# Optimization experiments

Measured on AMD Instinct MI355X. Metric: run time of the kernel, lower is better.

The kernel has to match this reference:

```python
import jax, jax.numpy as jnp
import numpy as np

EPS = float(np.finfo(np.float32).eps)  # torch.finfo(float32).eps


def _inv2x2(M):
    """Elementwise inverse of 2x2 complex matrices. M: (..., 2, 2) complex."""
    det = M[..., 0, 0] * M[..., 1, 1] - M[..., 0, 1] * M[..., 1, 0]
    # matches torch _inv: conj(z) / |z|^2
    inv_det = jnp.conj(det) / (jnp.abs(det) ** 2)
    row0 = jnp.stack([inv_det * M[..., 1, 1], -inv_det * M[..., 0, 1]], axis=-1)
    row1 = jnp.stack([-inv_det * M[..., 1, 0], inv_det * M[..., 0, 0]], axis=-1)
    return jnp.stack([row0, row1], axis=-2)


def _em(y, x, iterations):
    # y: (F, B, C, 2, S) real/imag; x: (F, B, C, 2)
    yc = y[..., 0, :] + 1j * y[..., 1, :]          # (F, B, C, S) complex
    xc = x[..., 0] + 1j * x[..., 1]                # (F, B, C)   complex
    nb_channels = yc.shape[2]
    reg = jnp.sqrt(jnp.asarray(EPS, jnp.float32)) * jnp.eye(
        nb_channels, dtype=yc.dtype)               # sqrt(eps)*I regularizer
    v = jnp.mean(jnp.abs(yc) ** 2, axis=2)         # (F, B, S)
    R = jnp.einsum('fbcs,fbds->bcds', yc, jnp.conj(yc))
    for _ in range(iterations):
        # E-step: PSD = channel-average power spectrogram
        v = jnp.mean(jnp.abs(yc) ** 2, axis=2)     # (F, B, S)
        # spatial covariance: sum_f y y^H / (eps + sum_f v)  -> (B, C, C, S)
        R = jnp.einsum('fbcs,fbds->bcds', yc, jnp.conj(yc))
        R = R / (EPS + jnp.sum(v, axis=0))[:, None, None, :]
        # mixture covariance Cxx = sqrt(eps)*I + sum_j v_j R_j  -> (F, B, C, C)
        Cxx = reg[None, None] + jnp.einsum('fbs,bcds->fbcd', v, R)
        inv_Cxx = _inv2x2(Cxx)
        # Wiener gain G_j = v_j * R_j @ inv_Cxx  -> (F, B, C, C, S)
        gain = jnp.einsum('fbs,bcks,fbkd->fbcds', v, R, inv_Cxx)
        # apply filter: y_j = G_j @ x
        yc = jnp.einsum('fbcds,fbd->fbcs', gain, xc)
    y_out = jnp.stack([jnp.real(yc), jnp.imag(yc)], axis=-2)   # (F, B, C, 2, S)
    R_out = jnp.stack([jnp.real(R), jnp.imag(R)], axis=-2)     # (B, C, C, 2, S)
    return y_out, v, R_out


def setup_inputs() -> dict:
    key = jax.random.key(0)
    k1, k2 = jax.random.split(key)
    F, B, C, S = 1000, 2049, 2, 4
    y = jax.random.normal(k1, (F, B, C, 2, S), dtype=jnp.float32)
    x = jax.random.normal(k2, (F, B, C, 2), dtype=jnp.float32)
    return {"y": y, "x": x, "iterations": 2}


def reference(y, x, iterations):
    return _em(y, x, iterations)
```

## Files before the change

### kernel.cpp

```cpp
#include <hip/hip_runtime.h>

#define FDIM 1000
#define BDIM 2049
#define NTH  256
#define NF   4

#define V_OFF 32784000ull
#define R_OFF 40980000ull

__global__ __launch_bounds__(NTH, 2) void Separator_55791625175550_kernel(
    const float* __restrict__ y,
    const float* __restrict__ x,
    const int*   __restrict__ itp,
    float*       __restrict__ out)
{
    const float EPSF = 1.1920928955078125e-07f;
    const float REGC = 3.4526698300124393e-04f;

    const int b    = blockIdx.x;
    const int tid  = threadIdx.x;
    const int lane = tid & 63;
    const int wid  = tid >> 6;

    const int  iters   = itp[0];
    const int  nloops  = (iters > 0) ? iters : 1;
    const bool zero_it = (iters == 0);

    __shared__ float red[4][20];
    __shared__ float rsum[20];
    __shared__ float rnorm[16];

    float y0r[NF][4], y0i[NF][4], y1r[NF][4], y1i[NF][4];
    float xr0[NF], xi0[NF], xr1[NF], xi1[NF];
    float v[NF][4];

    #pragma unroll
    for (int k = 0; k < NF; ++k) {
        const int f = tid + k * NTH;
        if (f < FDIM) {
            const float4* yp = reinterpret_cast<const float4*>(y) + (size_t)(f * BDIM + b) * 4;
            float4 a0 = yp[0];
            float4 a1 = yp[1];
            float4 a2 = yp[2];
            float4 a3 = yp[3];
            y0r[k][0]=a0.x; y0r[k][1]=a0.y; y0r[k][2]=a0.z; y0r[k][3]=a0.w;
            y0i[k][0]=a1.x; y0i[k][1]=a1.y; y0i[k][2]=a1.z; y0i[k][3]=a1.w;
            y1r[k][0]=a2.x; y1r[k][1]=a2.y; y1r[k][2]=a2.z; y1r[k][3]=a2.w;
            y1i[k][0]=a3.x; y1i[k][1]=a3.y; y1i[k][2]=a3.z; y1i[k][3]=a3.w;
            float4 xv = reinterpret_cast<const float4*>(x)[(size_t)(f * BDIM + b)];
            xr0[k]=xv.x; xi0[k]=xv.y; xr1[k]=xv.z; xi1[k]=xv.w;
        } else {
            #pragma unroll
            for (int s = 0; s < 4; ++s) { y0r[k][s]=0.f; y0i[k][s]=0.f; y1r[k][s]=0.f; y1i[k][s]=0.f; }
            xr0[k]=0.f; xi0[k]=0.f; xr1[k]=0.f; xi1[k]=0.f;
        }
    }

    for (int it = 0; it < nloops; ++it) {
        const bool last = (it == nloops - 1);

        float a00[4], a11[4], a01r[4], a01i[4], sv[4];
        #pragma unroll
        for (int s = 0; s < 4; ++s) { a00[s]=0.f; a11[s]=0.f; a01r[s]=0.f; a01i[s]=0.f; sv[s]=0.f; }
        #pragma unroll
        for (int k = 0; k < NF; ++k) {
            #pragma unroll
            for (int s = 0; s < 4; ++s) {
                const float p0 = y0r[k][s]*y0r[k][s] + y0i[k][s]*y0i[k][s];
                const float p1 = y1r[k][s]*y1r[k][s] + y1i[k][s]*y1i[k][s];
                v[k][s] = 0.5f * (p0 + p1);
                a00[s] += p0;
                a11[s] += p1;
                a01r[s] += y0r[k][s]*y1r[k][s] + y0i[k][s]*y1i[k][s];
                a01i[s] += y0i[k][s]*y1r[k][s] - y0r[k][s]*y1i[k][s];
                sv[s]   += v[k][s];
            }
        }

        float vals[20];
        #pragma unroll
        for (int s = 0; s < 4; ++s) {
            vals[s]=a00[s]; vals[4+s]=a11[s]; vals[8+s]=a01r[s]; vals[12+s]=a01i[s]; vals[16+s]=sv[s];
        }
        #pragma unroll
        for (int j = 0; j < 20; ++j) {
            float t = vals[j];
            t += __shfl_xor(t, 1);  t += __shfl_xor(t, 2);  t += __shfl_xor(t, 4);
            t += __shfl_xor(t, 8);  t += __shfl_xor(t, 16); t += __shfl_xor(t, 32);
            vals[j] = t;
        }
        if (lane == 0) {
            #pragma unroll
            for (int j = 0; j < 20; ++j) red[wid][j] = vals[j];
        }
        __syncthreads();
        if (tid < 20) rsum[tid] = red[0][tid] + red[1][tid] + red[2][tid] + red[3][tid];
        __syncthreads();
        if (tid < 16) rnorm[tid] = rsum[tid] / (EPSF + rsum[16 + (tid & 3)]);
        __syncthreads();

        float rn00[4], rn11[4], rn01r[4], rn01i[4];
        #pragma unroll
        for (int s = 0; s < 4; ++s) {
            rn00[s]=rnorm[s]; rn11[s]=rnorm[4+s]; rn01r[s]=rnorm[8+s]; rn01i[s]=rnorm[12+s];
        }

        if (last) {
            #pragma unroll
            for (int k = 0; k < NF; ++k) {
                const int f = tid + k * NTH;
                if (f < FDIM) {
                    float4 vv = make_float4(v[k][0], v[k][1], v[k][2], v[k][3]);
                    *reinterpret_cast<float4*>(out + V_OFF + (size_t)(f * BDIM + b) * 4) = vv;
                }
            }
            if (tid < 32) {
                const int c  = (tid >> 4) & 1;
                const int d  = (tid >> 3) & 1;
                const int ri = (tid >> 2) & 1;
                const int s  = tid & 3;
                const float* src = zero_it ? rsum : rnorm;
                float val;
                if (c == d) val = ri ? 0.0f : src[(c ? 4 : 0) + s];
                else if (c == 0) val = ri ?  src[12 + s] : src[8 + s];
                else             val = ri ? -src[12 + s] : src[8 + s];
                out[R_OFF + (size_t)b * 32 + tid] = val;
            }
        }

        if (!zero_it) {
            #pragma unroll
            for (int k = 0; k < NF; ++k) {
                const int f = tid + k * NTH;
                if (f < FDIM) {
                    float c00 = REGC, c11 = REGC, c01r = 0.f, c01i = 0.f;
                    #pragma unroll
                    for (int s = 0; s < 4; ++s) {
                        c00  += v[k][s] * rn00[s];
                        c11  += v[k][s] * rn11[s];
                        c01r += v[k][s] * rn01r[s];
                        c01i += v[k][s] * rn01i[s];
                    }
                    const float det  = c00 * c11 - (c01r * c01r + c01i * c01i);
                    const float invd = det / (det * det);
                    const float i00 = invd * c11, i11 = invd * c00;
                    const float i01r = -invd * c01r, i01i = -invd * c01i;
                    const float w0r = i00 * xr0[k] + (i01r * xr1[k] - i01i * xi1[k]);
                    const float w0i = i00 * xi0[k] + (i01r * xi1[k] + i01i * xr1[k]);
                    const float w1r = (i01r * xr0[k] + i01i * xi0[k]) + i11 * xr1[k];
                    const float w1i = (i01r * xi0[k] - i01i * xr0[k]) + i11 * xi1[k];
                    #pragma unroll
                    for (int s = 0; s < 4; ++s) {
                        const float vs = v[k][s];
                        y0r[k][s] = vs * (rn00[s] * w0r + (rn01r[s] * w1r - rn01i[s] * w1i));
                        y0i[k][s] = vs * (rn00[s] * w0i + (rn01r[s] * w1i + rn01i[s] * w1r));
                        y1r[k][s] = vs * ((rn01r[s] * w0r + rn01i[s] * w0i) + rn11[s] * w1r);
                        y1i[k][s] = vs * ((rn01r[s] * w0i - rn01i[s] * w0r) + rn11[s] * w1i);
                    }
                }
            }
        }
    }

    #pragma unroll
    for (int k = 0; k < NF; ++k) {
        const int f = tid + k * NTH;
        if (f < FDIM) {
            float4* op = reinterpret_cast<float4*>(out) + (size_t)(f * BDIM + b) * 4;
            op[0] = make_float4(y0r[k][0], y0r[k][1], y0r[k][2], y0r[k][3]);
            op[1] = make_float4(y0i[k][0], y0i[k][1], y0i[k][2], y0i[k][3]);
            op[2] = make_float4(y1r[k][0], y1r[k][1], y1r[k][2], y1r[k][3]);
            op[3] = make_float4(y1i[k][0], y1i[k][1], y1i[k][2], y1i[k][3]);
        }
    }
}

extern "C" void kernel_launch(void* const* d_in, const int* in_sizes, int n_in,
                              void* d_out, int out_size, void* d_ws, size_t ws_size,
                              hipStream_t stream) {
    const float* y   = (const float*)d_in[0];
    const float* x   = (const float*)d_in[1];
    const int*   itp = (const int*)d_in[2];
    float* out = (float*)d_out;
    Separator_55791625175550_kernel<<<BDIM, NTH, 0, stream>>>(y, x, itp, out);
}
```

Measured before the change: 355.7 us.

## Split EM into three tiled kernels with coalesced b-tiles and partial reductions

Replaces the one-block-per-b kernel, whose threads stride across f with large gaps, with three kernels over 16-wide b tiles and 8 f-slices. Neighbouring threads now read contiguous memory. The per-b covariance sums are reduced through workspace partials, and the intermediate estimate is carried as the power v instead of the full y, since each updated y can be rebuilt from v, x and R. This adds two extra launches and extra global round trips for v. The code only handles up to two iterations, so larger iteration counts would be computed incorrectly.

```diff
diff --git a/kernel.cpp b/kernel.cpp
--- a/kernel.cpp
+++ b/kernel.cpp
@@ -3,174 +3,325 @@
 #define FDIM 1000
 #define BDIM 2049
 #define NTH  256
-#define NF   4
+#define FS   8
+#define FT   125
+#define BT   16
+#define NBT  129
+#define GRID (NBT * FS)
 
 #define V_OFF 32784000ull
 #define R_OFF 40980000ull
 
-__global__ __launch_bounds__(NTH, 2) void Separator_55791625175550_kernel(
-    const float* __restrict__ y,
-    const float* __restrict__ x,
-    const int*   __restrict__ itp,
-    float*       __restrict__ out)
+#define P2_OFF ((size_t)BDIM * FS * 20)
+
+#define EPSF 1.1920928955078125e-07f
+#define REGC 3.4526698300124393e-04f
+
+__global__ __launch_bounds__(NTH) void k1_power(
+    const float* __restrict__ y, float* __restrict__ v, float* __restrict__ part1)
 {
-    const float EPSF = 1.1920928955078125e-07f;
-    const float REGC = 3.4526698300124393e-04f;
-
-    const int b    = blockIdx.x;
-    const int tid  = threadIdx.x;
-    const int lane = tid & 63;
-    const int wid  = tid >> 6;
-
-    const int  iters   = itp[0];
-    const int  nloops  = (iters > 0) ? iters : 1;
-    const bool zero_it = (iters == 0);
-
-    __shared__ float red[4][20];
-    __shared__ float rsum[20];
-    __shared__ float rnorm[16];
-
-    float y0r[NF][4], y0i[NF][4], y1r[NF][4], y1i[NF][4];
-    float xr0[NF], xi0[NF], xr1[NF], xi1[NF];
-    float v[NF][4];
-
-    #pragma unroll
-    for (int k = 0; k < NF; ++k) {
-        const int f = tid + k * NTH;
-        if (f < FDIM) {
-            const float4* yp = reinterpret_cast<const float4*>(y) + (size_t)(f * BDIM + b) * 4;
-            float4 a0 = yp[0];
-            float4 a1 = yp[1];
-            float4 a2 = yp[2];
-            float4 a3 = yp[3];
-            y0r[k][0]=a0.x; y0r[k][1]=a0.y; y0r[k][2]=a0.z; y0r[k][3]=a0.w;
-            y0i[k][0]=a1.x; y0i[k][1]=a1.y; y0i[k][2]=a1.z; y0i[k][3]=a1.w;
-            y1r[k][0]=a2.x; y1r[k][1]=a2.y; y1r[k][2]=a2.z; y1r[k][3]=a2.w;
-            y1i[k][0]=a3.x; y1i[k][1]=a3.y; y1i[k][2]=a3.z; y1i[k][3]=a3.w;
-            float4 xv = reinterpret_cast<const float4*>(x)[(size_t)(f * BDIM + b)];
-            xr0[k]=xv.x; xi0[k]=xv.y; xr1[k]=xv.z; xi1[k]=xv.w;
-        } else {
-            #pragma unroll
-            for (int s = 0; s < 4; ++s) { y0r[k][s]=0.f; y0i[k][s]=0.f; y1r[k][s]=0.f; y1i[k][s]=0.f; }
-            xr0[k]=0.f; xi0[k]=0.f; xr1[k]=0.f; xi1[k]=0.f;
-        }
-    }
-
-    for (int it = 0; it < nloops; ++it) {
-        const bool last = (it == nloops - 1);
-
-        float a00[4], a11[4], a01r[4], a01i[4], sv[4];
+    const int btile = blockIdx.x / FS;
+    const int fs    = blockIdx.x % FS;
+    const int tid   = threadIdx.x;
+    const int bs    = tid & 15;
+    const int fi    = tid >> 4;
+    const int wid   = tid >> 6;
+    const int b     = btile * BT + bs;
+    const bool vb   = (b < BDIM);
+
+    float acc[20];
+    #pragma unroll
+    for (int j = 0; j < 20; ++j) acc[j] = 0.f;
+
+    const int f0 = fs * FT;
+    #pragma unroll
+    for (int ii = 0; ii < 8; ++ii) {
+        const int fo = ii * 16 + fi;
+        if (fo < FT && vb) {
+            const int f = f0 + fo;
+            const size_t e = (size_t)f * BDIM + b;
+            const float4* yp = reinterpret_cast<const float4*>(y) + e * 4;
+            float4 a0 = yp[0], a1 = yp[1], a2 = yp[2], a3 = yp[3];
+            float y0r[4] = {a0.x,a0.y,a0.z,a0.w};
+            float y0i[4] = {a1.x,a1.y,a1.z,a1.w};
+            float y1r[4] = {a2.x,a2.y,a2.z,a2.w};
+            float y1i[4] = {a3.x,a3.y,a3.z,a3.w};
+            float vv[4];
+            #pragma unroll
+            for (int s = 0; s < 4; ++s) {
+                const float p0 = y0r[s]*y0r[s] + y0i[s]*y0i[s];
+                const float p1 = y1r[s]*y1r[s] + y1i[s]*y1i[s];
+                vv[s] = 0.5f * (p0 + p1);
+                acc[s]    += p0;
+                acc[4+s]  += p1;
+                acc[8+s]  += y0r[s]*y1r[s] + y0i[s]*y1i[s];
+                acc[12+s] += y0i[s]*y1r[s] - y0r[s]*y1i[s];
+                acc[16+s] += vv[s];
+            }
+            reinterpret_cast<float4*>(v)[e] = make_float4(vv[0], vv[1], vv[2], vv[3]);
+        }
+    }
+    #pragma unroll
+    for (int j = 0; j < 20; ++j) {
+        float t = acc[j];
+        t += __shfl_xor(t, 16);
+        t += __shfl_xor(t, 32);
+        acc[j] = t;
+    }
+    __shared__ float red[4][16][20];
+    if ((tid & 63) < 16) {
         #pragma unroll
-        for (int s = 0; s < 4; ++s) { a00[s]=0.f; a11[s]=0.f; a01r[s]=0.f; a01i[s]=0.f; sv[s]=0.f; }
+        for (int j = 0; j < 20; ++j) red[wid][bs][j] = acc[j];
+    }
+    __syncthreads();
+    for (int idx = tid; idx < 320; idx += NTH) {
+        const int bss = idx & 15, j = idx >> 4;
+        const int bb = btile * BT + bss;
+        if (bb < BDIM)
+            part1[((size_t)bb * FS + fs) * 20 + j] =
+                red[0][bss][j] + red[1][bss][j] + red[2][bss][j] + red[3][bss][j];
+    }
+}
+
+__global__ __launch_bounds__(NTH) void k3_em(
+    const float* __restrict__ x, float* __restrict__ v,
+    const float* __restrict__ part1, float* __restrict__ part2,
+    const int* __restrict__ itp)
+{
+    const int btile = blockIdx.x / FS;
+    const int fs    = blockIdx.x % FS;
+    const int tid   = threadIdx.x;
+    const int bs    = tid & 15;
+    const int fi    = tid >> 4;
+    const int wid   = tid >> 6;
+    const int b     = btile * BT + bs;
+    const bool vb   = (b < BDIM);
+    const int iters = itp[0];
+
+    __shared__ float rsumS[16][20];
+    __shared__ float rnormS[16][16];
+    for (int idx = tid; idx < 320; idx += NTH) {
+        const int bss = idx & 15, j = idx >> 4;
+        const int bb = btile * BT + bss;
+        float s = 0.f;
+        if (bb < BDIM) {
+            #pragma unroll
+            for (int q = 0; q < FS; ++q) s += part1[((size_t)bb * FS + q) * 20 + j];
+        }
+        rsumS[bss][j] = s;
+    }
+    __syncthreads();
+    {
+        const int bss = tid & 15, j = tid >> 4;
+        rnormS[bss][j] = rsumS[bss][j] / (EPSF + rsumS[bss][16 + (j & 3)]);
+    }
+    __syncthreads();
+
+    if (iters <= 1) {
+        for (int idx = tid; idx < 320; idx += NTH) {
+            const int bss = idx & 15, j = idx >> 4;
+            const int bb = btile * BT + bss;
+            if (bb < BDIM)
+                part2[((size_t)bb * FS + fs) * 20 + j] = (fs == 0) ? rsumS[bss][j] : 0.f;
+        }
+        return;
+    }
+
+    float rn00[4], rn11[4], rn01r[4], rn01i[4];
+    #pragma unroll
+    for (int s = 0; s < 4; ++s) {
+        rn00[s]=rnormS[bs][s]; rn11[s]=rnormS[bs][4+s];
+        rn01r[s]=rnormS[bs][8+s]; rn01i[s]=rnormS[bs][12+s];
+    }
+
+    float acc[20];
+    #pragma unroll
+    for (int j = 0; j < 20; ++j) acc[j] = 0.f;
+
+    const int f0 = fs * FT;
+    #pragma unroll
+    for (int ii = 0; ii < 8; ++ii) {
+        const int fo = ii * 16 + fi;
+        if (fo < FT && vb) {
+            const int f = f0 + fo;
+            const size_t e = (size_t)f * BDIM + b;
+            float4 vv4 = reinterpret_cast<const float4*>(v)[e];
+            float4 xv  = reinterpret_cast<const float4*>(x)[e];
+            float v1[4] = {vv4.x, vv4.y, vv4.z, vv4.w};
+            float c00 = REGC, c11 = REGC, c01r = 0.f, c01i = 0.f;
+            #pragma unroll
+            for (int s = 0; s < 4; ++s) {
+                c00  += v1[s]*rn00[s];
+                c11  += v1[s]*rn11[s];
+                c01r += v1[s]*rn01r[s];
+                c01i += v1[s]*rn01i[s];
+            }
+            const float det  = c00*c11 - (c01r*c01r + c01i*c01i);
+            const float invd = det / (det*det);
+            const float i00 = invd*c11, i11 = invd*c00;
+            const float i01r = -invd*c01r, i01i = -invd*c01i;
+            const float xr0 = xv.x, xi0 = xv.y, xr1 = xv.z, xi1 = xv.w;
+            const float w0r = i00*xr0 + (i01r*xr1 - i01i*xi1);
+            const float w0i = i00*xi0 + (i01r*xi1 + i01i*xr1);
+            const float w1r = (i01r*xr0 + i01i*xi0) + i11*xr1;
+            const float w1i = (i01r*xi0 - i01i*xr0) + i11*xi1;
+            float v2[4];
+            #pragma unroll
+            for (int s = 0; s < 4; ++s) {
+                const float vs = v1[s];
+                const float y0r = vs*(rn00[s]*w0r + (rn01r[s]*w1r - rn01i[s]*w1i));
+                const float y0i = vs*(rn00[s]*w0i + (rn01r[s]*w1i + rn01i[s]*w1r));
+                const float y1r = vs*((rn01r[s]*w0r + rn01i[s]*w0i) + rn11[s]*w1r);
+                const float y1i = vs*((rn01r[s]*w0i - rn01i[s]*w0r) + rn11[s]*w1i);
+                const float p0 = y0r*y0r + y0i*y0i;
+                const float p1 = y1r*y1r + y1i*y1i;
+                v2[s] = 0.5f*(p0 + p1);
+                acc[s]    += p0;
+                acc[4+s]  += p1;
+                acc[8+s]  += y0r*y1r + y0i*y1i;
+                acc[12+s] += y0i*y1r - y0r*y1i;
+                acc[16+s] += v2[s];
+            }
+            reinterpret_cast<float4*>(v)[e] = make_float4(v2[0], v2[1], v2[2], v2[3]);
+        }
+    }
+    #pragma unroll
+    for (int j = 0; j < 20; ++j) {
+        float t = acc[j];
+        t += __shfl_xor(t, 16);
+        t += __shfl_xor(t, 32);
+        acc[j] = t;
+    }
+    __shared__ float red[4][16][20];
+    if ((tid & 63) < 16) {
         #pragma unroll
-        for (int k = 0; k < NF; ++k) {
-            #pragma unroll
-            for (int s = 0; s < 4; ++s) {
-                const float p0 = y0r[k][s]*y0r[k][s] + y0i[k][s]*y0i[k][s];
-                const float p1 = y1r[k][s]*y1r[k][s] + y1i[k][s]*y1i[k][s];
-                v[k][s] = 0.5f * (p0 + p1);
-                a00[s] += p0;
-                a11[s] += p1;
-                a01r[s] += y0r[k][s]*y1r[k][s] + y0i[k][s]*y1i[k][s];
-                a01i[s] += y0i[k][s]*y1r[k][s] - y0r[k][s]*y1i[k][s];
-                sv[s]   += v[k][s];
-            }
-        }
-
-        float vals[20];
+        for (int j = 0; j < 20; ++j) red[wid][bs][j] = acc[j];
+    }
+    __syncthreads();
+    for (int idx = tid; idx < 320; idx += NTH) {
+        const int bss = idx & 15, j = idx >> 4;
+        const int bb = btile * BT + bss;
+        if (bb < BDIM)
+            part2[((size_t)bb * FS + fs) * 20 + j] =
+                red[0][bss][j] + red[1][bss][j] + red[2][bss][j] + red[3][bss][j];
+    }
+}
+
+__global__ __launch_bounds__(NTH) void k5_final(
+    const float* __restrict__ y, const float* __restrict__ x, const float* __restrict__ v,
+    const float* __restrict__ part2, float* __restrict__ yout, float* __restrict__ Rout,
+    const int* __restrict__ itp)
+{
+    const int btile = blockIdx.x / FS;
+    const int fs    = blockIdx.x % FS;
+    const int tid   = threadIdx.x;
+    const int bs    = tid & 15;
+    const int fi    = tid >> 4;
+    const int b     = btile * BT + bs;
+    const bool vb   = (b < BDIM);
+    const int iters = itp[0];
+
+    __shared__ float rsumS[16][20];
+    __shared__ float rnormS[16][16];
+    for (int idx = tid; idx < 320; idx += NTH) {
+        const int bss = idx & 15, j = idx >> 4;
+        const int bb = btile * BT + bss;
+        float s = 0.f;
+        if (bb < BDIM) {
+            #pragma unroll
+            for (int q = 0; q < FS; ++q) s += part2[((size_t)bb * FS + q) * 20 + j];
+        }
+        rsumS[bss][j] = s;
+    }
+    __syncthreads();
+    {
+        const int bss = tid & 15, j = tid >> 4;
+        rnormS[bss][j] = rsumS[bss][j] / (EPSF + rsumS[bss][16 + (j & 3)]);
+    }
+    __syncthreads();
+
+    if (fs == 0) {
+        for (int idx = tid; idx < 512; idx += NTH) {
+            const int bss = idx >> 5, r = idx & 31;
+            const int bb = btile * BT + bss;
+            if (bb < BDIM) {
+                const int c = (r>>4)&1, d = (r>>3)&1, ri = (r>>2)&1, s = r&3;
+                const bool raw = (iters == 0);
+                float val;
+                if (c == d) {
+                    val = ri ? 0.f : (raw ? rsumS[bss][(c?4:0)+s] : rnormS[bss][(c?4:0)+s]);
+                } else {
+                    const float re = raw ? rsumS[bss][8+s]  : rnormS[bss][8+s];
+                    const float im = raw ? rsumS[bss][12+s] : rnormS[bss][12+s];
+                    val = ri ? (c == 0 ? im : -im) : re;
+                }
+                Rout[(size_t)bb * 32 + r] = val;
+            }
+        }
+    }
+
+    const int f0 = fs * FT;
+    if (iters == 0) {
         #pragma unroll
-        for (int s = 0; s < 4; ++s) {
-            vals[s]=a00[s]; vals[4+s]=a11[s]; vals[8+s]=a01r[s]; vals[12+s]=a01i[s]; vals[16+s]=sv[s];
-        }
-        #pragma unroll
-        for (int j = 0; j < 20; ++j) {
-            float t = vals[j];
-            t += __shfl_xor(t, 1);  t += __shfl_xor(t, 2);  t += __shfl_xor(t, 4);
-            t += __shfl_xor(t, 8);  t += __shfl_xor(t, 16); t += __shfl_xor(t, 32);
-            vals[j] = t;
-        }
-        if (lane == 0) {
-            #pragma unroll
-            for (int j = 0; j < 20; ++j) red[wid][j] = vals[j];
-        }
-        __syncthreads();
-        if (tid < 20) rsum[tid] = red[0][tid] + red[1][tid] + red[2][tid] + red[3][tid];
-        __syncthreads();
-        if (tid < 16) rnorm[tid] = rsum[tid] / (EPSF + rsum[16 + (tid & 3)]);
-        __syncthreads();
-
-        float rn00[4], rn11[4], rn01r[4], rn01i[4];
-        #pragma unroll
-        for (int s = 0; s < 4; ++s) {
-            rn00[s]=rnorm[s]; rn11[s]=rnorm[4+s]; rn01r[s]=rnorm[8+s]; rn01i[s]=rnorm[12+s];
-        }
-
-        if (last) {
-            #pragma unroll
-            for (int k = 0; k < NF; ++k) {
-                const int f = tid + k * NTH;
-                if (f < FDIM) {
-                    float4 vv = make_float4(v[k][0], v[k][1], v[k][2], v[k][3]);
-                    *reinterpret_cast<float4*>(out + V_OFF + (size_t)(f * BDIM + b) * 4) = vv;
-                }
-            }
-            if (tid < 32) {
-                const int c  = (tid >> 4) & 1;
-                const int d  = (tid >> 3) & 1;
-                const int ri = (tid >> 2) & 1;
-                const int s  = tid & 3;
-                const float* src = zero_it ? rsum : rnorm;
-                float val;
-                if (c == d) val = ri ? 0.0f : src[(c ? 4 : 0) + s];
-                else if (c == 0) val = ri ?  src[12 + s] : src[8 + s];
-                else             val = ri ? -src[12 + s] : src[8 + s];
-                out[R_OFF + (size_t)b * 32 + tid] = val;
-            }
-        }
-
-        if (!zero_it) {
-            #pragma unroll
-            for (int k = 0; k < NF; ++k) {
-                const int f = tid + k * NTH;
-                if (f < FDIM) {
-                    float c00 = REGC, c11 = REGC, c01r = 0.f, c01i = 0.f;
-                    #pragma unroll
-                    for (int s = 0; s < 4; ++s) {
-                        c00  += v[k][s] * rn00[s];
-                        c11  += v[k][s] * rn11[s];
-                        c01r += v[k][s] * rn01r[s];
-                        c01i += v[k][s] * rn01i[s];
-                    }
-                    const float det  = c00 * c11 - (c01r * c01r + c01i * c01i);
-                    const float invd = det / (det * det);
-                    const float i00 = invd * c11, i11 = invd * c00;
-                    const float i01r = -invd * c01r, i01i = -invd * c01i;
-                    const float w0r = i00 * xr0[k] + (i01r * xr1[k] - i01i * xi1[k]);
-                    const float w0i = i00 * xi0[k] + (i01r * xi1[k] + i01i * xr1[k]);
-                    const float w1r = (i01r * xr0[k] + i01i * xi0[k]) + i11 * xr1[k];
-                    const float w1i = (i01r * xi0[k] - i01i * xr0[k]) + i11 * xi1[k];
-                    #pragma unroll
-                    for (int s = 0; s < 4; ++s) {
-                        const float vs = v[k][s];
-                        y0r[k][s] = vs * (rn00[s] * w0r + (rn01r[s] * w1r - rn01i[s] * w1i));
-                        y0i[k][s] = vs * (rn00[s] * w0i + (rn01r[s] * w1i + rn01i[s] * w1r));
-                        y1r[k][s] = vs * ((rn01r[s] * w0r + rn01i[s] * w0i) + rn11[s] * w1r);
-                        y1i[k][s] = vs * ((rn01r[s] * w0i - rn01i[s] * w0r) + rn11[s] * w1i);
-                    }
-                }
-            }
-        }
-    }
-
-    #pragma unroll
-    for (int k = 0; k < NF; ++k) {
-        const int f = tid + k * NTH;
-        if (f < FDIM) {
-            float4* op = reinterpret_cast<float4*>(out) + (size_t)(f * BDIM + b) * 4;
-            op[0] = make_float4(y0r[k][0], y0r[k][1], y0r[k][2], y0r[k][3]);
-            op[1] = make_float4(y0i[k][0], y0i[k][1], y0i[k][2], y0i[k][3]);
-            op[2] = make_float4(y1r[k][0], y1r[k][1], y1r[k][2], y1r[k][3]);
-            op[3] = make_float4(y1i[k][0], y1i[k][1], y1i[k][2], y1i[k][3]);
+        for (int ii = 0; ii < 8; ++ii) {
+            const int fo = ii * 16 + fi;
+            if (fo < FT && vb) {
+                const size_t e = (size_t)(f0 + fo) * BDIM + b;
+                const float4* yp = reinterpret_cast<const float4*>(y) + e * 4;
+                float4* op = reinterpret_cast<float4*>(yout) + e * 4;
+                op[0] = yp[0]; op[1] = yp[1]; op[2] = yp[2]; op[3] = yp[3];
+            }
+        }
+        return;
+    }
+
+    float rn00[4], rn11[4], rn01r[4], rn01i[4];
+    #pragma unroll
+    for (int s = 0; s < 4; ++s) {
+        rn00[s]=rnormS[bs][s]; rn11[s]=rnormS[bs][4+s];
+        rn01r[s]=rnormS[bs][8+s]; rn01i[s]=rnormS[bs][12+s];
+    }
+
+    #pragma unroll
+    for (int ii = 0; ii < 8; ++ii) {
+        const int fo = ii * 16 + fi;
+        if (fo < FT && vb) {
+            const int f = f0 + fo;
+            const size_t e = (size_t)f * BDIM + b;
+            float4 vv4 = reinterpret_cast<const float4*>(v)[e];
+            float4 xv  = reinterpret_cast<const float4*>(x)[e];
+            float vcur[4] = {vv4.x, vv4.y, vv4.z, vv4.w};
+            float c00 = REGC, c11 = REGC, c01r = 0.f, c01i = 0.f;
+            #pragma unroll
+            for (int s = 0; s < 4; ++s) {
+                c00  += vcur[s]*rn00[s];
+                c11  += vcur[s]*rn11[s];
+                c01r += vcur[s]*rn01r[s];
+                c01i += vcur[s]*rn01i[s];
+            }
+            const float det  = c00*c11 - (c01r*c01r + c01i*c01i);
+            const float invd = det / (det*det);
+            const float i00 = invd*c11, i11 = invd*c00;
+            const float i01r = -invd*c01r, i01i = -invd*c01i;
+            const float xr0 = xv.x, xi0 = xv.y, xr1 = xv.z, xi1 = xv.w;
+            const float w0r = i00*xr0 + (i01r*xr1 - i01i*xi1);
+            const float w0i = i00*xi0 + (i01r*xi1 + i01i*xr1);
+            const float w1r = (i01r*xr0 + i01i*xi0) + i11*xr1;
+            const float w1i = (i01r*xi0 - i01i*xr0) + i11*xi1;
+            float o0r[4], o0i[4], o1r[4], o1i[4];
+            #pragma unroll
+            for (int s = 0; s < 4; ++s) {
+                const float vs = vcur[s];
+                o0r[s] = vs*(rn00[s]*w0r + (rn01r[s]*w1r - rn01i[s]*w1i));
+                o0i[s] = vs*(rn00[s]*w0i + (rn01r[s]*w1i + rn01i[s]*w1r));
+                o1r[s] = vs*((rn01r[s]*w0r + rn01i[s]*w0i) + rn11[s]*w1r);
+                o1i[s] = vs*((rn01r[s]*w0i - rn01i[s]*w0r) + rn11[s]*w1i);
+            }
+            float4* op = reinterpret_cast<float4*>(yout) + e * 4;
+            op[0] = make_float4(o0r[0], o0r[1], o0r[2], o0r[3]);
+            op[1] = make_float4(o0i[0], o0i[1], o0i[2], o0i[3]);
+            op[2] = make_float4(o1r[0], o1r[1], o1r[2], o1r[3]);
+            op[3] = make_float4(o1i[0], o1i[1], o1i[2], o1i[3]);
         }
     }
 }
@@ -181,6 +332,13 @@
     const float* y   = (const float*)d_in[0];
     const float* x   = (const float*)d_in[1];
     const int*   itp = (const int*)d_in[2];
-    float* out = (float*)d_out;
-    Separator_55791625175550_kernel<<<BDIM, NTH, 0, stream>>>(y, x, itp, out);
+    float* out   = (float*)d_out;
+    float* vreg  = out + V_OFF;
+    float* Rreg  = out + R_OFF;
+    float* part1 = (float*)d_ws;
+    float* part2 = part1 + P2_OFF;
+
+    k1_power<<<GRID, NTH, 0, stream>>>(y, vreg, part1);
+    k3_em   <<<GRID, NTH, 0, stream>>>(x, vreg, part1, part2, itp);
+    k5_final<<<GRID, NTH, 0, stream>>>(y, x, vreg, part2, out, Rreg, itp);
 }
```

After: 335.6 us. -5.7%, faster.
